# Optimization experiments

Hardware: AMD Instinct MI355X
Metric: run time of the kernel (lower is better)

Reference implementation:

```python
import jax, jax.numpy as jnp
import numpy as np

NA_CUTOFF = 30.0
OTHER_CUTOFF = 15.0
THRESHOLDS = jnp.array([0.5, 1.0, 2.0, 4.0], dtype=jnp.float32)


def _cdist(x):
    # x: [b, n, 3] -> [b, n, n] euclidean distances, safe-sqrt (0 grad at 0)
    diff = x[:, :, None, :] - x[:, None, :, :]
    sq = jnp.sum(diff * diff, axis=-1)
    safe = jnp.where(sq > 0, sq, 1.0)
    return jnp.where(sq > 0, jnp.sqrt(safe), 0.0)


def setup_inputs() -> dict:
    key = jax.random.key(0)
    k1, k2, k3, k4, k5 = jax.random.split(key, 5)
    b, n = 2, 4096
    # angstrom-scale coordinates so cutoffs (15/30 A) are meaningful
    true_coords = jax.random.normal(k1, (b, n, 3), dtype=jnp.float32) * 20.0
    pred_coords = true_coords + jax.random.normal(k2, (b, n, 3), dtype=jnp.float32) * 1.0
    is_dna = jax.random.randint(k3, (b, n), 0, 2) > 0
    is_rna = jax.random.randint(k4, (b, n), 0, 2) > 0
    coords_mask = jax.random.randint(k5, (b, n), 0, 2) > 0
    return {
        'pred_coords': pred_coords,
        'true_coords': true_coords,
        'is_dna': is_dna,
        'is_rna': is_rna,
        'coords_mask': coords_mask,
    }


def reference(pred_coords, true_coords, is_dna, is_rna, coords_mask):
    b, n, _ = pred_coords.shape
    pred_dists = _cdist(pred_coords)            # [b, n, n]
    true_dists = _cdist(true_coords)            # [b, n, n]
    dist_diff = jnp.abs(true_dists - pred_dists)
    # eps: sigmoid(threshold - |d_true - d_pred|), averaged over 4 thresholds
    eps = jax.nn.sigmoid(THRESHOLDS - dist_diff[..., None]).mean(axis=-1)  # [b, n, n]

    is_nt = is_dna | is_rna
    nt_pair = is_nt[:, :, None] & is_nt[:, None, :]
    inclusion = jnp.where(nt_pair, true_dists < NA_CUTOFF, true_dists < OTHER_CUTOFF)
    mask = inclusion & ~jnp.eye(n, dtype=bool)[None]
    mask = mask & (coords_mask[:, :, None] & coords_mask[:, None, :])

    maskf = mask.astype(eps.dtype)
    num = (eps * maskf).sum(axis=(-1, -2))
    den = jnp.maximum(maskf.sum(axis=(-1, -2)), 1.0)
    lddt = num / den
    return 1.0 - lddt.mean()
```

## Files before the change

### kernel.cpp

```cpp
#include <hip/hip_runtime.h>
#include <math.h>

#define TS 64
#define NTHREADS 256
#define JPT 16
#define LUTN 512
#define LUT_DMAX 12.0f
#define LUT_SCALE ((float)LUTN / LUT_DMAX)
#define S_DIAG 3.2163287777874683f

typedef float v2f __attribute__((ext_vector_type(2)));

__device__ __forceinline__ float fsqrt(float x) {
#if __has_builtin(__builtin_amdgcn_sqrtf)
    return __builtin_amdgcn_sqrtf(x);
#else
    return sqrtf(x);
#endif
}

__device__ __forceinline__ float sig4(float d) {
    const float e = expf(d);
    return 1.0f / (1.0f + e * 0.60653065971263342360f)
         + 1.0f / (1.0f + e * 0.36787944117144232160f)
         + 1.0f / (1.0f + e * 0.13533528323661269189f)
         + 1.0f / (1.0f + e * 0.01831563888873418029f);
}

__device__ __forceinline__ void pair_tail(float sqp, float sqt, float cut,
                                          const float2* __restrict__ lut,
                                          float& num, float& den) {
    const float dp = fsqrt(sqp);
    const float dt = fsqrt(sqt);
    float u = fabsf(dt - dp) * LUT_SCALE;
    u = fminf(u, (float)LUTN - 0.001f);
    const int idx = (int)u;
    const float fr = u - (float)idx;
    const float2 L = lut[idx];
    const float s = fmaf(fr, L.y, L.x);
    const float m = (dt < cut) ? 1.0f : 0.0f;
    num = fmaf(m, s, num);
    den += m;
}

__global__ __launch_bounds__(NTHREADS) void lddt_tile_kernel(
    const float* __restrict__ pred, const float* __restrict__ tru,
    const int* __restrict__ is_dna, const int* __restrict__ is_rna,
    const int* __restrict__ cmask,
    float* __restrict__ pnum, float* __restrict__ pden,
    int n, int T, int nslots)
{
    __shared__ __align__(16) float sPX[TS], sPY[TS], sPZ[TS];
    __shared__ __align__(16) float sTX[TS], sTY[TS], sTZ[TS];
    __shared__ __align__(16) float sCut[2 * TS];
    __shared__ float2 sLUT[LUTN];
    __shared__ float wnum[4], wden[4];

    const int tid = threadIdx.x;

    int slot = blockIdx.x;
    const int bi = slot / nslots;
    slot -= bi * nslots;
    const int W = 2 * T + 1;
    int ti = (int)(((float)W - fsqrt((float)(W * W - 8 * slot))) * 0.5f);
    while ((ti + 1) * (W - (ti + 1)) / 2 <= slot) ++ti;
    while (ti * (W - ti) / 2 > slot) --ti;
    const int tj = ti + (slot - ti * (W - ti) / 2);
    const bool diag = (ti == tj);
    const int i0 = ti * TS, j0 = tj * TS;
    const size_t base = (size_t)bi * n;

    if (tid < TS) {
        const int j = j0 + tid;
        const float* p = pred + (base + j) * 3;
        const float* q = tru  + (base + j) * 3;
        sPX[tid] = p[0]; sPY[tid] = p[1]; sPZ[tid] = p[2];
        sTX[tid] = q[0]; sTY[tid] = q[1]; sTZ[tid] = q[2];
        const bool ntj = (is_dna[base + j] != 0) || (is_rna[base + j] != 0);
        const bool cmj = (cmask[base + j] != 0);
        sCut[tid]      = cmj ? (ntj ? 30.0f : 15.0f) : 0.0f;
        sCut[TS + tid] = cmj ? 15.0f : 0.0f;
    }

    for (int e = tid; e < LUTN; e += NTHREADS) {
        const float d0 = (float)e * (LUT_DMAX / LUTN);
        const float f0 = sig4(d0);
        const float f1 = sig4(d0 + (LUT_DMAX / LUTN));
        sLUT[e] = make_float2(f0, f1 - f0);
    }

    const int il = tid & (TS - 1);
    const int i  = i0 + il;
    const float* p = pred + (base + i) * 3;
    const float* q = tru  + (base + i) * 3;
    const float pix = p[0], piy = p[1], piz = p[2];
    const float tix = q[0], tiy = q[1], tiz = q[2];
    const bool nti = (is_dna[base + i] != 0) || (is_rna[base + i] != 0);
    const float cmf = (cmask[base + i] != 0) ? 1.0f : 0.0f;
    __syncthreads();

    const float* cutsel = nti ? &sCut[0] : &sCut[TS];
    const int kbase = (tid >> 6) * JPT;

    float num = 0.0f, den = 0.0f;
    const v2f px2 = {pix, pix}, py2 = {piy, piy}, pz2 = {piz, piz};
    const v2f tx2 = {tix, tix}, ty2 = {tiy, tiy}, tz2 = {tiz, tiz};

    #pragma unroll
    for (int qd = 0; qd < JPT / 4; ++qd) {
        const int jq = kbase + 4 * qd;
        const float4 PX = *(const float4*)&sPX[jq];
        const float4 PY = *(const float4*)&sPY[jq];
        const float4 PZ = *(const float4*)&sPZ[jq];
        const float4 TX = *(const float4*)&sTX[jq];
        const float4 TY = *(const float4*)&sTY[jq];
        const float4 TZ = *(const float4*)&sTZ[jq];
        const float4 CT = *(const float4*)&cutsel[jq];

        v2f dx, dy, dz, sqpA, sqpB, sqtA, sqtB;

        dx = px2 - (v2f){PX.x, PX.y}; dy = py2 - (v2f){PY.x, PY.y}; dz = pz2 - (v2f){PZ.x, PZ.y};
        sqpA = dx * dx + dy * dy + dz * dz;
        dx = tx2 - (v2f){TX.x, TX.y}; dy = ty2 - (v2f){TY.x, TY.y}; dz = tz2 - (v2f){TZ.x, TZ.y};
        sqtA = dx * dx + dy * dy + dz * dz;

        dx = px2 - (v2f){PX.z, PX.w}; dy = py2 - (v2f){PY.z, PY.w}; dz = pz2 - (v2f){PZ.z, PZ.w};
        sqpB = dx * dx + dy * dy + dz * dz;
        dx = tx2 - (v2f){TX.z, TX.w}; dy = ty2 - (v2f){TY.z, TY.w}; dz = tz2 - (v2f){TZ.z, TZ.w};
        sqtB = dx * dx + dy * dy + dz * dz;

        pair_tail(sqpA.x, sqtA.x, CT.x, sLUT, num, den);
        pair_tail(sqpA.y, sqtA.y, CT.y, sLUT, num, den);
        pair_tail(sqpB.x, sqtB.x, CT.z, sLUT, num, den);
        pair_tail(sqpB.y, sqtB.y, CT.w, sLUT, num, den);
    }

    num *= cmf;
    den *= cmf;
    if (diag && tid < TS) {
        num -= cmf * S_DIAG;
        den -= cmf;
    }

    #pragma unroll
    for (int off = 32; off > 0; off >>= 1) {
        num += __shfl_down(num, off, 64);
        den += __shfl_down(den, off, 64);
    }
    const int w = tid >> 6;
    if ((tid & 63) == 0) { wnum[w] = num; wden[w] = den; }
    __syncthreads();

    if (tid == 0) {
        const float tn = wnum[0] + wnum[1] + wnum[2] + wnum[3];
        const float td = wden[0] + wden[1] + wden[2] + wden[3];
        pnum[blockIdx.x] = diag ? tn : tn * 2.0f;
        pden[blockIdx.x] = diag ? td : td * 2.0f;
    }
}

__global__ __launch_bounds__(256) void lddt_final_kernel(
    const float* __restrict__ pnum, const float* __restrict__ pden,
    float* __restrict__ out, int nslots)
{
    __shared__ double sn0[4], sn1[4], sd0[4], sd1[4];
    double n0 = 0, n1 = 0, d0 = 0, d1 = 0;
    for (int s = threadIdx.x; s < 2 * nslots; s += 256) {
        if (s < nslots) { n0 += (double)pnum[s]; d0 += (double)pden[s]; }
        else            { n1 += (double)pnum[s]; d1 += (double)pden[s]; }
    }
    #pragma unroll
    for (int off = 32; off > 0; off >>= 1) {
        n0 += __shfl_down(n0, off, 64); d0 += __shfl_down(d0, off, 64);
        n1 += __shfl_down(n1, off, 64); d1 += __shfl_down(d1, off, 64);
    }
    const int w = threadIdx.x >> 6;
    if ((threadIdx.x & 63) == 0) { sn0[w] = n0; sn1[w] = n1; sd0[w] = d0; sd1[w] = d1; }
    __syncthreads();
    if (threadIdx.x == 0) {
        double N0 = sn0[0] + sn0[1] + sn0[2] + sn0[3];
        double N1 = sn1[0] + sn1[1] + sn1[2] + sn1[3];
        double D0 = sd0[0] + sd0[1] + sd0[2] + sd0[3];
        double D1 = sd1[0] + sd1[1] + sd1[2] + sd1[3];
        D0 = D0 > 1.0 ? D0 : 1.0;
        D1 = D1 > 1.0 ? D1 : 1.0;
        const double l0 = 0.25 * N0 / D0;
        const double l1 = 0.25 * N1 / D1;
        out[0] = (float)(1.0 - 0.5 * (l0 + l1));
    }
}

extern "C" void kernel_launch(void* const* d_in, const int* in_sizes, int n_in,
                              void* d_out, int out_size, void* d_ws, size_t ws_size,
                              hipStream_t stream) {
    const float* pred = (const float*)d_in[0];
    const float* tru  = (const float*)d_in[1];
    const int*   dna  = (const int*)d_in[2];
    const int*   rna  = (const int*)d_in[3];
    const int*   cm   = (const int*)d_in[4];
    float* out = (float*)d_out;

    const int B = 2;
    const int n = in_sizes[2] / B;
    const int T = n / TS;
    const int nslots = T * (T + 1) / 2;

    float* pnum = (float*)d_ws;
    float* pden = (float*)((char*)d_ws + (size_t)B * nslots * sizeof(float));

    const int grid = B * nslots;

    hipLaunchKernelGGL(lddt_tile_kernel, dim3(grid), dim3(NTHREADS), 0, stream,
                       pred, tru, dna, rna, cm, pnum, pden, n, T, nslots);
    hipLaunchKernelGGL(lddt_final_kernel, dim3(1), dim3(256), 0, stream,
                       pnum, pden, out, nslots);
}
```

Baseline: 85.81 us.

## Index sigmoid LUT by squared distance difference via float exponent bits

Replaces the two per-pair square roots with one sqrt of the product, computing (dt-dp)^2 = sqt+sqp-2*sqrt(sqt*sqp). The lookup table is now indexed by the float bit pattern of that squared difference, giving log-spaced octaves with linear sub-buckets, so index and fraction come from bit shifts instead of a float-to-int conversion. Cutoffs are compared in squared space. This cuts transcendental and conversion instructions in the inner loop. It risks cancellation error when the squared difference is small, and a larger LUT to build per block.

```diff
diff --git a/kernel.cpp b/kernel.cpp
--- a/kernel.cpp
+++ b/kernel.cpp
@@ -4,10 +4,13 @@
 #define TS 64
 #define NTHREADS 256
 #define JPT 16
-#define LUTN 512
-#define LUT_DMAX 12.0f
-#define LUT_SCALE ((float)LUTN / LUT_DMAX)
-#define S_DIAG 3.2163287777874683f
+
+#define LUTN 768
+#define OCT_LO (-16)
+#define U_MIN 1.52587890625e-5f
+#define U_MAX 255.999f
+#define IDX_BIAS 28416u
+#define FRAC_SCALE 3.814697265625e-6f
 
 typedef float v2f __attribute__((ext_vector_type(2)));
 
@@ -18,6 +21,13 @@
     return sqrtf(x);
 #endif
 }
+__device__ __forceinline__ float fmed3(float x, float lo, float hi) {
+#if __has_builtin(__builtin_amdgcn_fmed3f)
+    return __builtin_amdgcn_fmed3f(x, lo, hi);
+#else
+    return fminf(fmaxf(x, lo), hi);
+#endif
+}
 
 __device__ __forceinline__ float sig4(float d) {
     const float e = expf(d);
@@ -27,18 +37,17 @@
          + 1.0f / (1.0f + e * 0.01831563888873418029f);
 }
 
-__device__ __forceinline__ void pair_tail(float sqp, float sqt, float cut,
-                                          const float2* __restrict__ lut,
+__device__ __forceinline__ void pair_tail(float sqp, float sqt, float cut2,
+                                          const char* __restrict__ lutB,
                                           float& num, float& den) {
-    const float dp = fsqrt(sqp);
-    const float dt = fsqrt(sqt);
-    float u = fabsf(dt - dp) * LUT_SCALE;
-    u = fminf(u, (float)LUTN - 0.001f);
-    const int idx = (int)u;
-    const float fr = u - (float)idx;
-    const float2 L = lut[idx];
-    const float s = fmaf(fr, L.y, L.x);
-    const float m = (dt < cut) ? 1.0f : 0.0f;
+    const float r  = fsqrt(sqt * sqp);
+    const float u0 = fmaf(-2.0f, r, sqt + sqp);
+    const float u  = fmed3(u0, U_MIN, U_MAX);
+    const unsigned int bits = __float_as_uint(u);
+    const float2 L = *(const float2*)(lutB + ((bits >> 15) & ~7u));
+    const float fr = (float)(bits & 0x3FFFFu) * FRAC_SCALE;
+    const float s  = fmaf(fr, L.y, L.x);
+    const float m  = (sqt < cut2) ? 1.0f : 0.0f;
     num = fmaf(m, s, num);
     den += m;
 }
@@ -78,14 +87,18 @@
         sTX[tid] = q[0]; sTY[tid] = q[1]; sTZ[tid] = q[2];
         const bool ntj = (is_dna[base + j] != 0) || (is_rna[base + j] != 0);
         const bool cmj = (cmask[base + j] != 0);
-        sCut[tid]      = cmj ? (ntj ? 30.0f : 15.0f) : 0.0f;
-        sCut[TS + tid] = cmj ? 15.0f : 0.0f;
+        sCut[tid]      = cmj ? (ntj ? 900.0f : 225.0f) : 0.0f;
+        sCut[TS + tid] = cmj ? 225.0f : 0.0f;
     }
 
     for (int e = tid; e < LUTN; e += NTHREADS) {
-        const float d0 = (float)e * (LUT_DMAX / LUTN);
-        const float f0 = sig4(d0);
-        const float f1 = sig4(d0 + (LUT_DMAX / LUTN));
+        const int oct = e >> 5;
+        const int k   = e & 31;
+        const float base2 = exp2f((float)(oct + OCT_LO));
+        const float u0 = base2 * (1.0f + (float)k * 0.03125f);
+        const float u1 = u0 + base2 * 0.03125f;
+        const float f0 = sig4(fsqrt(u0));
+        const float f1 = sig4(fsqrt(u1));
         sLUT[e] = make_float2(f0, f1 - f0);
     }
 
@@ -100,6 +113,7 @@
     __syncthreads();
 
     const float* cutsel = nti ? &sCut[0] : &sCut[TS];
+    const char* lutB = (const char*)sLUT - IDX_BIAS;
     const int kbase = (tid >> 6) * JPT;
 
     float num = 0.0f, den = 0.0f;
@@ -129,16 +143,16 @@
         dx = tx2 - (v2f){TX.z, TX.w}; dy = ty2 - (v2f){TY.z, TY.w}; dz = tz2 - (v2f){TZ.z, TZ.w};
         sqtB = dx * dx + dy * dy + dz * dz;
 
-        pair_tail(sqpA.x, sqtA.x, CT.x, sLUT, num, den);
-        pair_tail(sqpA.y, sqtA.y, CT.y, sLUT, num, den);
-        pair_tail(sqpB.x, sqtB.x, CT.z, sLUT, num, den);
-        pair_tail(sqpB.y, sqtB.y, CT.w, sLUT, num, den);
+        pair_tail(sqpA.x, sqtA.x, CT.x, lutB, num, den);
+        pair_tail(sqpA.y, sqtA.y, CT.y, lutB, num, den);
+        pair_tail(sqpB.x, sqtB.x, CT.z, lutB, num, den);
+        pair_tail(sqpB.y, sqtB.y, CT.w, lutB, num, den);
     }
 
     num *= cmf;
     den *= cmf;
     if (diag && tid < TS) {
-        num -= cmf * S_DIAG;
+        num -= cmf * sig4(0.00390625f);
         den -= cmf;
     }
 
```

New measurement: 91.33 us. 6.4% more time.
